# Kernel tuning notes

Hardware: AMD Instinct MI355X
Metric: run time of the kernel (lower is better)

Reference implementation:

```python
import math
import jax, jax.numpy as jnp
import numpy as np

B, L, DM = 2, 1024, 1024
STATE, EXPAND, CONV, DTR = 16, 2, 4, 8
INNER = DM * EXPAND          # 2048
NFFT = L // 2 + 1            # 513


def _silu(v):
    return v * jax.nn.sigmoid(v)


def setup_inputs() -> dict:
    key = jax.random.key(0)
    ks = jax.random.split(key, 12)
    s = lambda k, shape, sc=0.02: (jax.random.normal(k, shape, jnp.float32) * sc)
    # dt_proj bias initialized like the torch module: exp(U(0,1)*(log dt_max - log dt_min) + log dt_min)
    inv_dt = jnp.exp(jax.random.uniform(ks[10], (INNER,), jnp.float32)
                     * (math.log(0.1) - math.log(0.001)) + math.log(0.001))
    return {
        "x": jax.random.normal(ks[0], (B, L, DM), jnp.float32),
        "in_proj_w": s(ks[1], (2 * INNER, DM)),
        "conv_w": s(ks[2], (INNER, 1, CONV), 0.1),      # depthwise conv kernel
        "conv_b": jnp.zeros((INNER,), jnp.float32),
        "A_log": jnp.tile(jnp.log(jnp.arange(1, STATE + 1, dtype=jnp.float32)), (INNER, 1)),
        "D": jnp.ones((INNER,), jnp.float32),
        "x_proj_w": s(ks[3], (DTR + 2 * STATE, INNER)),
        "dt_proj_w": s(ks[4], (INNER, DTR)),
        "dt_proj_b": inv_dt,
        "filter_real": s(ks[5], (INNER, NFFT)),
        "filter_imag": s(ks[6], (INNER, NFFT)),
        "spectral_decay": jnp.ones((INNER,), jnp.float32) * 0.01,
        "fusion_w": s(ks[7], (INNER, 2 * INNER)),
        "fusion_b": jnp.zeros((INNER,), jnp.float32),
        "out_proj_w": s(ks[8], (DM, INNER)),
        "ln_gamma": jnp.ones((DM,), jnp.float32),
        "ln_beta": jnp.zeros((DM,), jnp.float32),
    }


def reference(x, in_proj_w, conv_w, conv_b, A_log, D, x_proj_w, dt_proj_w, dt_proj_b,
              filter_real, filter_imag, spectral_decay, fusion_w, fusion_b,
              out_proj_w, ln_gamma, ln_beta):
    residual = x
    xz = x @ in_proj_w.T                                   # [B,L,2*INNER]
    x_inner, z = xz[..., :INNER], xz[..., INNER:]
    z = _silu(z)

    # ---- SSM path ----
    xc = jnp.swapaxes(x_inner, 1, 2)                       # [B,E,L]
    xc = jax.lax.conv_general_dilated(
        xc, conv_w, (1,), [(CONV - 1, 0)],                 # causal depthwise conv (pad-left == torch pad + truncate)
        dimension_numbers=("NCH", "OIH", "NCH"),
        feature_group_count=INNER) + conv_b[None, :, None]
    x_conv = jnp.swapaxes(_silu(xc), 1, 2)                 # [B,L,E]

    x_dbc = x_conv @ x_proj_w.T                            # [B,L,DTR+2S]
    dt_x = x_dbc[..., :DTR]
    Bm = x_dbc[..., DTR:DTR + STATE]                       # [B,L,S]
    Cm = x_dbc[..., DTR + STATE:]                          # [B,L,S]
    dt = jax.nn.softplus(dt_x @ dt_proj_w.T + dt_proj_b)   # [B,L,E]
    A = -jnp.exp(A_log)                                    # [E,S]
    dA = jnp.exp(dt[..., None] * A)                        # [B,L,E,S]
    dBx = (dt * x_conv)[..., None] * Bm[:, :, None, :]     # [B,L,E,S]

    def step(h, inp):
        dA_t, dBx_t, C_t = inp
        h = dA_t * h + dBx_t                               # [B,E,S]
        return h, jnp.einsum('bes,bs->be', h, C_t)

    h0 = jnp.zeros((B, INNER, STATE), x.dtype)
    _, ys = jax.lax.scan(step, h0,
                         (jnp.swapaxes(dA, 0, 1), jnp.swapaxes(dBx, 0, 1), jnp.swapaxes(Cm, 0, 1)))
    y_ssm = jnp.swapaxes(ys, 0, 1) + x_conv * D            # [B,L,E]

    # ---- Spectral path ----
    xf = jnp.fft.rfft(jnp.swapaxes(x_inner, 1, 2), axis=-1)        # [B,E,NFFT]
    freqs = jnp.linspace(0.0, 1.0, NFFT)
    filt = (filter_real + 1j * filter_imag) * jnp.exp(-spectral_decay[:, None] * freqs[None, :])
    y_spec = jnp.swapaxes(jnp.fft.irfft(xf * filt[None], n=L, axis=-1), 1, 2)  # [B,L,E]

    # ---- Gated fusion ----
    g = jax.nn.sigmoid(jnp.concatenate([y_ssm, y_spec], -1) @ fusion_w.T + fusion_b)
    y = g * y_ssm + (1.0 - g) * y_spec
    y = y * z
    out = y @ out_proj_w.T + residual                      # [B,L,DM]

    mu = out.mean(-1, keepdims=True)
    var = out.var(-1, keepdims=True)
    return (out - mu) / jnp.sqrt(var + 1e-5) * ln_gamma + ln_beta
```

## Files before the change

### kernel.cpp

```cpp
#include <hip/hip_runtime.h>
#include <math.h>

#define B_ 2
#define L_ 1024
#define DM_ 1024
#define STATE_ 16
#define CONV_ 4
#define DTR_ 8
#define INNER_ 2048
#define M_ (B_*L_)
#define MD_ (B_*INNER_)
#define NFFT_ 513
#define NFP_ 1088
#define NCH_ 32
#define CHL_ 32
#define SK_ 16
#define KSL_ (2048/SK_)

typedef unsigned short u16;
typedef __attribute__((ext_vector_type(8))) short short8;
typedef __attribute__((ext_vector_type(8))) __bf16 bf16x8;
typedef __attribute__((ext_vector_type(4))) float f32x4;

__device__ __forceinline__ float frcp_(float x) { return __builtin_amdgcn_rcpf(x); }
__device__ __forceinline__ float fexp_(float x) { return __expf(x); }
__device__ __forceinline__ float fsigm_(float x) { return frcp_(1.f + __expf(-x)); }
__device__ __forceinline__ float fsilu_(float x) { return x * frcp_(1.f + __expf(-x)); }
__device__ __forceinline__ float fsoftplus_(float v) {
  return (v > 20.f) ? v : __logf(1.f + __expf(v));
}
__device__ __forceinline__ u16 f2bf(float f) {
  union { float f; unsigned u; } v; v.f = f;
  unsigned r = v.u + 0x7fffu + ((v.u >> 16) & 1u);
  return (u16)(r >> 16);
}
__device__ __forceinline__ float bf2f(u16 h) {
  union { unsigned u; float f; } v; v.u = ((unsigned)h) << 16;
  return v.f;
}
__device__ __forceinline__ void gload16(const void* g, void* l) {
  __builtin_amdgcn_global_load_lds(
      (const __attribute__((address_space(1))) unsigned*)g,
      (__attribute__((address_space(3))) unsigned*)l, 16, 0, 0);
}
__device__ __forceinline__ f32x4 mfma_bf16(short8 a, short8 b, f32x4 c) {
  return __builtin_amdgcn_mfma_f32_16x16x32_bf16(
      __builtin_bit_cast(bf16x8, a), __builtin_bit_cast(bf16x8, b), c, 0, 0, 0);
}

#define CVT2_N0 2097152
#define CVT2_NT 6291456
__global__ __launch_bounds__(256) void cvt2_k(
    const float* __restrict__ s0, const float* __restrict__ s1,
    u16* __restrict__ out)
{
  int i = (blockIdx.x*256 + threadIdx.x) * 4;
  const float* src; int off;
  if (i < CVT2_N0) { src = s0; off = 0; }
  else             { src = s1; off = CVT2_N0; }
  float4 v = *(const float4*)(src + (i - off));
  ushort4 o;
  o.x = f2bf(v.x); o.y = f2bf(v.y); o.z = f2bf(v.z); o.w = f2bf(v.w);
  *(ushort4*)(out + i) = o;
}

__device__ __forceinline__ void cvt16_body(int eb, int nthr, int t,
    const float* __restrict__ src, u16* __restrict__ dst)
{
  int i = (eb*nthr + t)*16;
  #pragma unroll
  for (int q = 0; q < 4; q++) {
    float4 v = *(const float4*)(src + i + q*4);
    ushort4 o;
    o.x = f2bf(v.x); o.y = f2bf(v.y); o.z = f2bf(v.z); o.w = f2bf(v.w);
    *(ushort4*)(dst + i + q*4) = o;
  }
}

__device__ __forceinline__ void conv_xt_body(int idx, const float* __restrict__ xz,
    const float* __restrict__ cw, const float* __restrict__ cb,
    float* __restrict__ xc, u16* __restrict__ xt)
{
  int c = idx & (INNER_-1);
  int g = idx >> 11;
  int b = g >> 7;
  int lb = (g & 127) * 8;
  float w0=cw[c*4+0], w1=cw[c*4+1], w2=cw[c*4+2], w3=cw[c*4+3];
  float bias = cb[c];
  float v[11];
  #pragma unroll
  for (int j = 0; j < 11; j++) {
    int l = lb - 3 + j;
    v[j] = (l >= 0) ? xz[((size_t)((b << 10) + l))*4096 + c] : 0.f;
  }
  union { u16 a[8]; short8 v8; } tu;
  #pragma unroll
  for (int j = 0; j < 8; j++) tu.a[j] = f2bf(v[j+3]);
  *(short8*)&xt[(((size_t)(b*INNER_ + c)) << 10) + lb] = tu.v8;
  #pragma unroll
  for (int j = 0; j < 8; j++) {
    float s = bias + w0*v[j] + w1*v[j+1] + w2*v[j+2] + w3*v[j+3];
    xc[((size_t)((b << 10) + lb + j))*INNER_ + c] = fsilu_(s);
  }
}

__device__ __forceinline__ void genWdft_body(int idx, u16* __restrict__ W)
{
  int l = idx & (L_-1);
  int col = idx >> 10;
  float v = 0.f;
  int f = col >> 1;
  if (f < NFFT_) {
    int ph = (l*f) & (L_-1);
    float th = (float)ph * (6.283185307179586f / (float)L_);
    v = (col & 1) ? -__sinf(th) : __cosf(th);
  }
  W[idx] = f2bf(v);
}

__device__ __forceinline__ void genWinv_body(int idx, u16* __restrict__ W)
{
  int r = idx % NFP_;
  int l = idx / NFP_;
  int f = r >> 1;
  float v = 0.f;
  if (f < NFFT_) {
    bool edge = (f == 0) || (f == 512);
    float sc = (edge ? 1.f : 2.f) / (float)L_;
    int ph = (f*l) & (L_-1);
    float th = (float)ph * (6.283185307179586f / (float)L_);
    if (r & 1) v = edge ? 0.f : -sc*__sinf(th);
    else       v = sc*__cosf(th);
  }
  W[idx] = f2bf(v);
}

__device__ __forceinline__ void xproj_body(int eb,
    const float* __restrict__ xconv, const float* __restrict__ W,
    float* __restrict__ part)
{
  const int sk = eb & (SK_-1), mt = eb / SK_;
  const int k0 = sk*KSL_;
  const int m = mt*256 + threadIdx.x;
  const float* arow = xconv + (size_t)m*2048 + k0;
  const float* wrow = W + k0;
  float acc[40];
  #pragma unroll
  for (int j=0;j<40;j++) acc[j]=0.f;
  for (int k = 0; k < KSL_; k += 4) {
    float4 a = *(const float4*)(arow + k);
    #pragma unroll
    for (int j = 0; j < 40; j++) {
      float4 b = *(const float4*)(wrow + (size_t)j*2048 + k);
      acc[j] += a.x*b.x + a.y*b.y + a.z*b.z + a.w*b.w;
    }
  }
  float* o = part + ((size_t)sk*M_ + m)*40;
  #pragma unroll
  for (int j = 0; j < 10; j++)
    *(float4*)(o + j*4) = make_float4(acc[j*4], acc[j*4+1], acc[j*4+2], acc[j*4+3]);
}

__device__ __forceinline__ void xpred_body(int i, const float* __restrict__ part,
                                           float* __restrict__ xdbc)
{
  float s = 0.f;
  #pragma unroll
  for (int sk = 0; sk < SK_; sk++) s += part[(size_t)sk*81920 + i];
  xdbc[i] = s;
}

__global__ __launch_bounds__(256) void aux2_k(
    const float* __restrict__ xz, const float* __restrict__ cw,
    const float* __restrict__ cb, float* __restrict__ xc,
    u16* __restrict__ xt, u16* __restrict__ Winv,
    const float* __restrict__ ows, u16* __restrict__ owd)
{
  int eb = blockIdx.x;
  if (eb < 2048)      conv_xt_body(eb*256 + threadIdx.x, xz, cw, cb, xc, xt);
  else if (eb < 6400) genWinv_body((eb - 2048)*256 + threadIdx.x, Winv);
  else                cvt16_body(eb - 6400, 256, threadIdx.x, ows, owd);
}

template<int TM, int TN, int EPI, int YCH, int AUX, int KS>
__global__ __launch_bounds__((TM/64)*(TN/32)*64) void mgemm_k(
    const u16* __restrict__ Ab, const u16* __restrict__ Bb,
    void* __restrict__ Cout, int K, int ldc,
    const float* __restrict__ aux0, u16* __restrict__ aux1,
    const float* __restrict__ aux2, const float* __restrict__ aux3,
    int gx, int gy,
    const float* __restrict__ ga, const float* __restrict__ gb,
    float* __restrict__ go, u16* __restrict__ gw,
    int ldk, const float* __restrict__ cvs, u16* __restrict__ cvd)
{
  constexpr int WN   = TN/32;
  constexpr int NW   = (TM/64)*WN;
  constexpr int NTHR = NW*64;
  __shared__ __align__(16) u16 As[2][TM*64];
  __shared__ __align__(16) u16 Bs[2][TN*64];
  const int t = threadIdx.x;
  const int nwg = gx * gy;

  if constexpr (AUX != 0) {
    int eb = (int)blockIdx.x - nwg*KS;
    if (eb >= 0) {
      if constexpr (AUX == 1) {
        if (eb < 2176) genWdft_body(eb*NTHR + t, gw);
        else           cvt16_body(eb - 2176, NTHR, t, cvs, cvd);
      } else if constexpr (AUX == 3) {
        xproj_body(eb, ga, gb, go);
      } else {
        xpred_body(eb*256 + t, ga, go);
      }
      return;
    }
  }

  const int lane = t & 63;
  const int w = t >> 6;
  const int wm = w / WN, wn = w % WN;

  int bid = blockIdx.x;
  int ks = 0;
  if constexpr (KS > 1) { ks = bid / nwg; bid -= ks*nwg; }
  const int k0 = ks * K;
  const int lid = (bid & 7) * (nwg >> 3) + (bid >> 3);
  int bx, by;
  if (YCH) { by = lid / gx; bx = lid - by*gx; }
  else     { bx = lid / gy; by = lid - bx*gy; }
  const int M0 = by * TM, N0 = bx * TN;

  f32x4 acc[4][2] = {};

  auto stage = [&](int buf, int kk0) {
    #pragma unroll
    for (int q = 0; q < TM*8/NTHR; q++) {
      int u = q*NTHR + t;
      int row = u >> 3, gpr = u & 7;
      int grp = gpr ^ (row & 7);
      gload16(Ab + (size_t)(M0+row)*ldk + k0 + kk0 + grp*8, &As[buf][u*8]);
    }
    #pragma unroll
    for (int q = 0; q < TN*8/NTHR; q++) {
      int u = q*NTHR + t;
      int row = u >> 3, gpr = u & 7;
      int grp = gpr ^ (row & 7);
      gload16(Bb + (size_t)(N0+row)*ldk + k0 + kk0 + grp*8, &Bs[buf][u*8]);
    }
  };

  stage(0, 0);
  const int nk = K >> 6;
  for (int kst = 0; kst < nk; kst++) {
    const int buf = kst & 1;
    __syncthreads();
    if (kst + 1 < nk) stage(buf ^ 1, (kst + 1) << 6);
    const u16* Asb = As[buf];
    const u16* Bsb = Bs[buf];
    #pragma unroll
    for (int kk = 0; kk < 2; kk++) {
      const int quad = lane >> 4;
      const int grp = kk*4 + quad;
      short8 af[4], bfr[2];
      #pragma unroll
      for (int i = 0; i < 4; i++) {
        int row = wm*64 + i*16 + (lane & 15);
        af[i] = *(const short8*)&Asb[(row*8 + (grp ^ (row & 7)))*8];
      }
      #pragma unroll
      for (int j = 0; j < 2; j++) {
        int row = wn*32 + j*16 + (lane & 15);
        bfr[j] = *(const short8*)&Bsb[(row*8 + (grp ^ (row & 7)))*8];
      }
      #pragma unroll
      for (int i = 0; i < 4; i++)
        #pragma unroll
        for (int j = 0; j < 2; j++)
          acc[i][j] = mfma_bf16(af[i], bfr[j], acc[i][j]);
    }
  }

  if constexpr (EPI == 6) {
    u16* T = (u16*)&As[0][0];
    __syncthreads();
    #pragma unroll
    for (int i = 0; i < 4; i++) {
      int cb = wm*64 + i*16 + (lane >> 4)*4;
      #pragma unroll
      for (int j = 0; j < 2; j++) {
        int ll = wn*32 + j*16 + (lane & 15);
        #pragma unroll
        for (int r = 0; r < 4; r++)
          T[(cb + r)*66 + ll] = f2bf(acc[i][j][r]);
      }
    }
    __syncthreads();
    const int b2 = M0 >> 11, c0 = M0 & (INNER_-1);
    u16* yc = (u16*)Cout;
    #pragma unroll
    for (int q = 0; q < (TM*TN/8)/NTHR; q++) {
      int task = q*NTHR + t;
      int cg = task & 15, ll = task >> 4;
      union { u16 a[8]; short8 v8; } tu;
      #pragma unroll
      for (int e = 0; e < 8; e++) tu.a[e] = T[(cg*8 + e)*66 + ll];
      *(short8*)&yc[((size_t)((b2 << 10) + N0 + ll) << 12) + 2048 + c0 + cg*8] = tu.v8;
    }
  } else {
    #pragma unroll
    for (int i = 0; i < 4; i++) {
      int mbase = M0 + wm*64 + i*16 + (lane >> 4)*4;
      #pragma unroll
      for (int j = 0; j < 2; j++) {
        int n = N0 + wn*32 + j*16 + (lane & 15);
        #pragma unroll
        for (int r = 0; r < 4; r++) {
          int m = mbase + r;
          float v = acc[i][j][r];
          if (EPI == 0) {
            ((float*)Cout)[(size_t)m*ldc + n] = v;
          } else if (EPI == 3) {
            float pv = __shfl_xor(v, 1, 64);
            int f = n >> 1;
            float outv = 0.f;
            if (f < NFFT_) {
              int c = m & (INNER_-1);
              float d  = fexp_(-aux2[c] * (float)f * (1.f/512.f));
              float wr = aux0[c*NFFT_+f]*d, wi = aux3[c*NFFT_+f]*d;
              float a = (n & 1) ? pv : v;
              float b = (n & 1) ? v : pv;
              outv = (n & 1) ? (a*wi + b*wr) : (a*wr - b*wi);
            }
            ((u16*)Cout)[(size_t)m*ldc + n] = f2bf(outv);
          } else if (EPI == 7) {
            float* P = (float*)Cout + (size_t)ks * ((size_t)gy*TM*ldc);
            P[(size_t)m*ldc + n] = v;
          } else {
            u16* P = (u16*)Cout + (size_t)ks * ((size_t)gy*TM*ldc);
            P[(size_t)m*ldc + n] = f2bf(v);
          }
        }
      }
    }
  }
}

__global__ __launch_bounds__(256) void combine_gate_k(
    const u16* __restrict__ P, const float* __restrict__ fus_b,
    const u16* __restrict__ ycat, const float* __restrict__ xz,
    u16* __restrict__ ycomb)
{
  int i4 = (blockIdx.x*256 + threadIdx.x)*4;
  int m = i4 >> 11, n = i4 & 2047;
  ushort4 p0 = *(const ushort4*)(P + i4);
  ushort4 p1 = *(const ushort4*)(P + 4194304 + i4);
  ushort4 ysv = *(const ushort4*)(ycat + (size_t)m*4096 + n);
  ushort4 ypv = *(const ushort4*)(ycat + (size_t)m*4096 + 2048 + n);
  float4 zv = *(const float4*)(xz + (size_t)m*4096 + 2048 + n);
  float4 fb = *(const float4*)(fus_b + n);
  float pp[4] = {bf2f(p0.x)+bf2f(p1.x), bf2f(p0.y)+bf2f(p1.y),
                 bf2f(p0.z)+bf2f(p1.z), bf2f(p0.w)+bf2f(p1.w)};
  float zz[4] = {zv.x, zv.y, zv.z, zv.w};
  float bb[4] = {fb.x, fb.y, fb.z, fb.w};
  u16 ys[4] = {ysv.x, ysv.y, ysv.z, ysv.w};
  u16 yp[4] = {ypv.x, ypv.y, ypv.z, ypv.w};
  ushort4 o;
  u16* op = (u16*)&o;
  #pragma unroll
  for (int j = 0; j < 4; j++) {
    float g = fsigm_(pp[j] + bb[j]);
    op[j] = f2bf((g*bf2f(ys[j]) + (1.f-g)*bf2f(yp[j]))*fsilu_(zz[j]));
  }
  *(ushort4*)(ycomb + i4) = o;
}

__global__ __launch_bounds__(256) void scan1_k(
    const float* __restrict__ xdbc, const float* __restrict__ xconv,
    const float* __restrict__ A_log, const float* __restrict__ dtw,
    const float* __restrict__ dtb, float* __restrict__ Pq)
{
  int idx = blockIdx.x*256 + threadIdx.x;
  int e  = idx & (INNER_-1);
  int bc = idx >> 11;
  int ch = bc & (NCH_-1);
  int b  = bc >> 5;
  float A[STATE_];
  #pragma unroll
  for (int s=0;s<STATE_;s++) A[s] = -fexp_(A_log[e*STATE_+s]);
  float w[DTR_];
  #pragma unroll
  for (int r=0;r<DTR_;r++) w[r] = dtw[e*DTR_+r];
  float bias = dtb[e];
  float h[STATE_] = {};
  float sdt = 0.f;
  int mbase = b*L_ + ch*CHL_;
  float dtx[DTR_], Bv[STATE_], xcv;
  {
    const float* row = xdbc + (size_t)mbase*40;
    #pragma unroll
    for (int r=0;r<DTR_;r++) dtx[r] = row[r];
    #pragma unroll
    for (int s=0;s<STATE_;s++) Bv[s] = row[8+s];
    xcv = xconv[(size_t)mbase*INNER_ + e];
  }
  for (int l=0;l<CHL_;l++) {
    float ndtx[DTR_], nBv[STATE_], nxcv = 0.f;
    if (l+1 < CHL_) {
      const float* nrow = xdbc + (size_t)(mbase+l+1)*40;
      #pragma unroll
      for (int r=0;r<DTR_;r++) ndtx[r] = nrow[r];
      #pragma unroll
      for (int s=0;s<STATE_;s++) nBv[s] = nrow[8+s];
      nxcv = xconv[(size_t)(mbase+l+1)*INNER_ + e];
    } else {
      #pragma unroll
      for (int r=0;r<DTR_;r++) ndtx[r] = 0.f;
      #pragma unroll
      for (int s=0;s<STATE_;s++) nBv[s] = 0.f;
    }
    float v = bias;
    #pragma unroll
    for (int r=0;r<DTR_;r++) v += dtx[r]*w[r];
    float dt = fsoftplus_(v);
    sdt += dt;
    float dx = dt * xcv;
    #pragma unroll
    for (int s=0;s<STATE_;s++) {
      float dA = fexp_(dt*A[s]);
      h[s] = dA*h[s] + dx*Bv[s];
    }
    #pragma unroll
    for (int r=0;r<DTR_;r++) dtx[r] = ndtx[r];
    #pragma unroll
    for (int s=0;s<STATE_;s++) Bv[s] = nBv[s];
    xcv = nxcv;
  }
  float* o = Pq + (size_t)idx*32;
  #pragma unroll
  for (int s=0;s<STATE_;s++) { o[s] = fexp_(A[s]*sdt); o[16+s] = h[s]; }
}

__global__ __launch_bounds__(256) void scan2_k(float* __restrict__ Pq)
{
  int idx = blockIdx.x*256 + threadIdx.x;
  int s = idx & 15;
  int e = (idx >> 4) & (INNER_-1);
  int b = idx >> 15;
  float h = 0.f;
  for (int ch = 0; ch < NCH_; ch++) {
    size_t base = ((size_t)(b*NCH_+ch)*INNER_ + e)*32;
    float p = Pq[base + s];
    float q = Pq[base + 16 + s];
    Pq[base + 16 + s] = h;
    h = p*h + q;
  }
}

__global__ __launch_bounds__(256) void scan3_k(
    const float* __restrict__ xdbc, const float* __restrict__ xconv,
    const float* __restrict__ A_log, const float* __restrict__ dtw,
    const float* __restrict__ dtb, const float* __restrict__ Dp,
    const float* __restrict__ Pq, u16* __restrict__ ycat)
{
  int idx = blockIdx.x*256 + threadIdx.x;
  int e  = idx & (INNER_-1);
  int bc = idx >> 11;
  int ch = bc & (NCH_-1);
  int b  = bc >> 5;
  float A[STATE_];
  #pragma unroll
  for (int s=0;s<STATE_;s++) A[s] = -fexp_(A_log[e*STATE_+s]);
  float w[DTR_];
  #pragma unroll
  for (int r=0;r<DTR_;r++) w[r] = dtw[e*DTR_+r];
  float bias = dtb[e];
  float Dv = Dp[e];
  float h[STATE_];
  const float* hi = Pq + (size_t)idx*32 + 16;
  #pragma unroll
  for (int s=0;s<STATE_;s++) h[s] = hi[s];
  int mbase = b*L_ + ch*CHL_;
  float dtx[DTR_], Bv[STATE_], Cv[STATE_], xcv;
  {
    const float* row = xdbc + (size_t)mbase*40;
    #pragma unroll
    for (int r=0;r<DTR_;r++) dtx[r] = row[r];
    #pragma unroll
    for (int s=0;s<STATE_;s++) { Bv[s] = row[8+s]; Cv[s] = row[24+s]; }
    xcv = xconv[(size_t)mbase*INNER_ + e];
  }
  for (int l=0;l<CHL_;l++) {
    float ndtx[DTR_], nBv[STATE_], nCv[STATE_], nxcv = 0.f;
    if (l+1 < CHL_) {
      const float* nrow = xdbc + (size_t)(mbase+l+1)*40;
      #pragma unroll
      for (int r=0;r<DTR_;r++) ndtx[r] = nrow[r];
      #pragma unroll
      for (int s=0;s<STATE_;s++) { nBv[s] = nrow[8+s]; nCv[s] = nrow[24+s]; }
      nxcv = xconv[(size_t)(mbase+l+1)*INNER_ + e];
    } else {
      #pragma unroll
      for (int r=0;r<DTR_;r++) ndtx[r] = 0.f;
      #pragma unroll
      for (int s=0;s<STATE_;s++) { nBv[s] = 0.f; nCv[s] = 0.f; }
    }
    float v = bias;
    #pragma unroll
    for (int r=0;r<DTR_;r++) v += dtx[r]*w[r];
    float dt = fsoftplus_(v);
    float dx = dt * xcv;
    float y = 0.f;
    #pragma unroll
    for (int s=0;s<STATE_;s++) {
      float dA = fexp_(dt*A[s]);
      h[s] = dA*h[s] + dx*Bv[s];
      y += h[s]*Cv[s];
    }
    ycat[(size_t)(mbase+l)*4096 + e] = f2bf(y + xcv*Dv);
    #pragma unroll
    for (int r=0;r<DTR_;r++) dtx[r] = ndtx[r];
    #pragma unroll
    for (int s=0;s<STATE_;s++) { Bv[s] = nBv[s]; Cv[s] = nCv[s]; }
    xcv = nxcv;
  }
}

__global__ __launch_bounds__(256) void ln2_k(const float* __restrict__ Q,
    const float* __restrict__ xres,
    const float* __restrict__ gma, const float* __restrict__ bta,
    float* __restrict__ out)
{
  int m = blockIdx.x;
  float s=0.f, s2=0.f;
  float v[4];
  #pragma unroll
  for (int j=0;j<4;j++) {
    int n = threadIdx.x + j*256;
    size_t idx = (size_t)m*DM_ + n;
    v[j] = Q[idx] + Q[2097152 + idx] + xres[idx];
    s += v[j]; s2 += v[j]*v[j];
  }
  #pragma unroll
  for (int off=32; off>=1; off>>=1) {
    s  += __shfl_down(s, off);
    s2 += __shfl_down(s2, off);
  }
  __shared__ float rs[4], rs2[4], stats[2];
  int wid = threadIdx.x >> 6;
  if ((threadIdx.x & 63) == 0) { rs[wid]=s; rs2[wid]=s2; }
  __syncthreads();
  if (threadIdx.x == 0) {
    float ts  = rs[0]+rs[1]+rs[2]+rs[3];
    float ts2 = rs2[0]+rs2[1]+rs2[2]+rs2[3];
    float mu  = ts/(float)DM_;
    float var = ts2/(float)DM_ - mu*mu;
    stats[0] = mu; stats[1] = rsqrtf(var + 1e-5f);
  }
  __syncthreads();
  float mu = stats[0], rstd = stats[1];
  #pragma unroll
  for (int j=0;j<4;j++) {
    int n = threadIdx.x + j*256;
    out[(size_t)m*DM_ + n] = (v[j]-mu)*rstd*gma[n] + bta[n];
  }
}

extern "C" void kernel_launch(void* const* d_in, const int* in_sizes, int n_in,
                              void* d_out, int out_size, void* d_ws, size_t ws_size,
                              hipStream_t stream)
{
  const float* x       = (const float*)d_in[0];
  const float* in_w    = (const float*)d_in[1];
  const float* conv_w  = (const float*)d_in[2];
  const float* conv_b  = (const float*)d_in[3];
  const float* A_log   = (const float*)d_in[4];
  const float* Dp      = (const float*)d_in[5];
  const float* xproj_w = (const float*)d_in[6];
  const float* dt_w    = (const float*)d_in[7];
  const float* dt_b    = (const float*)d_in[8];
  const float* f_re    = (const float*)d_in[9];
  const float* f_im    = (const float*)d_in[10];
  const float* s_dec   = (const float*)d_in[11];
  const float* fus_w   = (const float*)d_in[12];
  const float* fus_b   = (const float*)d_in[13];
  const float* out_w   = (const float*)d_in[14];
  const float* ln_g    = (const float*)d_in[15];
  const float* ln_b    = (const float*)d_in[16];
  float* out = (float*)d_out;

  float* ws    = (float*)d_ws;
  float* xz    = ws;
  float* xconv = xz    + 8388608;
  float* xdbc  = xconv + 4194304;
  float* Pq    = xdbc  + 81920;
  u16* ub      = (u16*)(Pq + 4194304);
  u16* xb      = ub;
  u16* inwb    = xb    + 2097152;
  u16* fuswb   = inwb  + 4194304;
  u16* outwb   = fuswb + 8388608;
  u16* xt      = outwb + 2097152;
  u16* Wb      = xt    + 4194304;
  u16* XFb     = Wb    + 1114112;
  u16* ycat    = XFb   + 4456448;
  u16* ycomb   = xt;
  u16* Winv    = xb;
  float* part  = (float*)inwb;
  u16* fpart   = (u16*)xconv;
  float* opart = Pq;

  cvt2_k<<<CVT2_NT/1024, 256, 0, stream>>>(x, in_w, xb);

  mgemm_k<128,128,0,0,1,1><<<512 + 2176 + 1024, 512, 0, stream>>>(
      xb, inwb, xz, 1024, 4096, nullptr, nullptr, nullptr, nullptr, 32, 16,
      nullptr, nullptr, nullptr, Wb, 1024, fus_w, fuswb);
  aux2_k<<<6912, 256, 0, stream>>>(xz, conv_w, conv_b, xconv, xt, Winv, out_w, outwb);
  mgemm_k<128,64,3,1,3,1><<<544 + SK_*8, 256, 0, stream>>>(
      xt, Wb, XFb, 1024, NFP_, f_re, nullptr, s_dec, f_im, 17, 32,
      xconv, xproj_w, part, nullptr, 1024, nullptr, nullptr);
  mgemm_k<128,64,6,1,4,1><<<512 + 320, 256, 0, stream>>>(
      XFb, Winv, ycat, NFP_, 0, nullptr, nullptr, nullptr, nullptr, 16, 32,
      part, nullptr, xdbc, nullptr, NFP_, nullptr, nullptr);
  scan1_k<<<(B_*NCH_*INNER_)/256, 256, 0, stream>>>(xdbc, xconv, A_log, dt_w, dt_b, Pq);
  scan2_k<<<(B_*INNER_*STATE_)/256, 256, 0, stream>>>(Pq);
  scan3_k<<<(B_*NCH_*INNER_)/256, 256, 0, stream>>>(xdbc, xconv, A_log, dt_w, dt_b, Dp, Pq, ycat);
  mgemm_k<128,128,8,0,0,2><<<2*256, 512, 0, stream>>>(
      ycat, fuswb, fpart, 2048, 2048, nullptr, nullptr, nullptr, nullptr, 16, 16,
      nullptr, nullptr, nullptr, nullptr, 4096, nullptr, nullptr);
  combine_gate_k<<<(2048*2048/4)/256, 256, 0, stream>>>(
      fpart, fus_b, ycat, xz, ycomb);
  mgemm_k<64,64,7,1,0,2><<<2*512, 128, 0, stream>>>(
      ycomb, outwb, opart, 1024, 1024, nullptr, nullptr, nullptr, nullptr, 16, 32,
      nullptr, nullptr, nullptr, nullptr, 2048, nullptr, nullptr);
  ln2_k<<<M_, 256, 0, stream>>>(opart, x, ln_g, ln_b, out);
}
```

Before: 399.1 us.

## Compute x_proj with bf16 MFMA GEMM instead of fp32 split-K scalar path

```diff
diff --git a/kernel.cpp b/kernel.cpp
--- a/kernel.cpp
+++ b/kernel.cpp
@@ -14,8 +14,6 @@
 #define NFP_ 1088
 #define NCH_ 32
 #define CHL_ 32
-#define SK_ 16
-#define KSL_ (2048/SK_)
 
 typedef unsigned short u16;
 typedef __attribute__((ext_vector_type(8))) short short8;
@@ -135,51 +133,18 @@
   W[idx] = f2bf(v);
 }
 
-__device__ __forceinline__ void xproj_body(int eb,
-    const float* __restrict__ xconv, const float* __restrict__ W,
-    float* __restrict__ part)
-{
-  const int sk = eb & (SK_-1), mt = eb / SK_;
-  const int k0 = sk*KSL_;
-  const int m = mt*256 + threadIdx.x;
-  const float* arow = xconv + (size_t)m*2048 + k0;
-  const float* wrow = W + k0;
-  float acc[40];
-  #pragma unroll
-  for (int j=0;j<40;j++) acc[j]=0.f;
-  for (int k = 0; k < KSL_; k += 4) {
-    float4 a = *(const float4*)(arow + k);
-    #pragma unroll
-    for (int j = 0; j < 40; j++) {
-      float4 b = *(const float4*)(wrow + (size_t)j*2048 + k);
-      acc[j] += a.x*b.x + a.y*b.y + a.z*b.z + a.w*b.w;
-    }
-  }
-  float* o = part + ((size_t)sk*M_ + m)*40;
-  #pragma unroll
-  for (int j = 0; j < 10; j++)
-    *(float4*)(o + j*4) = make_float4(acc[j*4], acc[j*4+1], acc[j*4+2], acc[j*4+3]);
-}
-
-__device__ __forceinline__ void xpred_body(int i, const float* __restrict__ part,
-                                           float* __restrict__ xdbc)
-{
-  float s = 0.f;
-  #pragma unroll
-  for (int sk = 0; sk < SK_; sk++) s += part[(size_t)sk*81920 + i];
-  xdbc[i] = s;
-}
-
 __global__ __launch_bounds__(256) void aux2_k(
     const float* __restrict__ xz, const float* __restrict__ cw,
     const float* __restrict__ cb, float* __restrict__ xc,
     u16* __restrict__ xt, u16* __restrict__ Winv,
-    const float* __restrict__ ows, u16* __restrict__ owd)
+    const float* __restrict__ ows, u16* __restrict__ owd,
+    const float* __restrict__ xpws, u16* __restrict__ xpwd)
 {
   int eb = blockIdx.x;
   if (eb < 2048)      conv_xt_body(eb*256 + threadIdx.x, xz, cw, cb, xc, xt);
   else if (eb < 6400) genWinv_body((eb - 2048)*256 + threadIdx.x, Winv);
-  else                cvt16_body(eb - 6400, 256, threadIdx.x, ows, owd);
+  else if (eb < 6912) cvt16_body(eb - 6400, 256, threadIdx.x, ows, owd);
+  else                cvt16_body(eb - 6912, 256, threadIdx.x, xpws, xpwd);
 }
 
 template<int TM, int TN, int EPI, int YCH, int AUX, int KS>
@@ -189,8 +154,7 @@
     const float* __restrict__ aux0, u16* __restrict__ aux1,
     const float* __restrict__ aux2, const float* __restrict__ aux3,
     int gx, int gy,
-    const float* __restrict__ ga, const float* __restrict__ gb,
-    float* __restrict__ go, u16* __restrict__ gw,
+    u16* __restrict__ gw,
     int ldk, const float* __restrict__ cvs, u16* __restrict__ cvd)
 {
   constexpr int WN   = TN/32;
@@ -207,10 +171,8 @@
       if constexpr (AUX == 1) {
         if (eb < 2176) genWdft_body(eb*NTHR + t, gw);
         else           cvt16_body(eb - 2176, NTHR, t, cvs, cvd);
-      } else if constexpr (AUX == 3) {
-        xproj_body(eb, ga, gb, go);
       } else {
-        xpred_body(eb*256 + t, ga, go);
+        cvt16_body(eb, NTHR, t, cvs, cvd);
       }
       return;
     }
@@ -335,9 +297,11 @@
           } else if (EPI == 7) {
             float* P = (float*)Cout + (size_t)ks * ((size_t)gy*TM*ldc);
             P[(size_t)m*ldc + n] = v;
-          } else {
+          } else if (EPI == 8) {
             u16* P = (u16*)Cout + (size_t)ks * ((size_t)gy*TM*ldc);
             P[(size_t)m*ldc + n] = f2bf(v);
+          } else {
+            if (n < 40) ((float*)Cout)[(size_t)m*40 + n] = v;
           }
         }
       }
@@ -604,7 +568,8 @@
   u16* ycat    = XFb   + 4456448;
   u16* ycomb   = xt;
   u16* Winv    = xb;
-  float* part  = (float*)inwb;
+  u16* xpwb    = xb + 1114112;
+  u16* xcb     = inwb;
   u16* fpart   = (u16*)xconv;
   float* opart = Pq;
 
@@ -612,24 +577,28 @@
 
   mgemm_k<128,128,0,0,1,1><<<512 + 2176 + 1024, 512, 0, stream>>>(
       xb, inwb, xz, 1024, 4096, nullptr, nullptr, nullptr, nullptr, 32, 16,
-      nullptr, nullptr, nullptr, Wb, 1024, fus_w, fuswb);
-  aux2_k<<<6912, 256, 0, stream>>>(xz, conv_w, conv_b, xconv, xt, Winv, out_w, outwb);
-  mgemm_k<128,64,3,1,3,1><<<544 + SK_*8, 256, 0, stream>>>(
+      Wb, 1024, fus_w, fuswb);
+  aux2_k<<<6932, 256, 0, stream>>>(xz, conv_w, conv_b, xconv, xt, Winv,
+                                   out_w, outwb, xproj_w, xpwb);
+  mgemm_k<128,64,3,1,3,1><<<544 + 1024, 256, 0, stream>>>(
       xt, Wb, XFb, 1024, NFP_, f_re, nullptr, s_dec, f_im, 17, 32,
-      xconv, xproj_w, part, nullptr, 1024, nullptr, nullptr);
-  mgemm_k<128,64,6,1,4,1><<<512 + 320, 256, 0, stream>>>(
+      nullptr, 1024, xconv, xcb);
+  mgemm_k<128,64,9,1,0,1><<<16, 256, 0, stream>>>(
+      xcb, xpwb, xdbc, 2048, 40, nullptr, nullptr, nullptr, nullptr, 1, 16,
+      nullptr, 2048, nullptr, nullptr);
+  mgemm_k<128,64,6,1,0,1><<<512, 256, 0, stream>>>(
       XFb, Winv, ycat, NFP_, 0, nullptr, nullptr, nullptr, nullptr, 16, 32,
-      part, nullptr, xdbc, nullptr, NFP_, nullptr, nullptr);
+      nullptr, NFP_, nullptr, nullptr);
   scan1_k<<<(B_*NCH_*INNER_)/256, 256, 0, stream>>>(xdbc, xconv, A_log, dt_w, dt_b, Pq);
   scan2_k<<<(B_*INNER_*STATE_)/256, 256, 0, stream>>>(Pq);
   scan3_k<<<(B_*NCH_*INNER_)/256, 256, 0, stream>>>(xdbc, xconv, A_log, dt_w, dt_b, Dp, Pq, ycat);
   mgemm_k<128,128,8,0,0,2><<<2*256, 512, 0, stream>>>(
       ycat, fuswb, fpart, 2048, 2048, nullptr, nullptr, nullptr, nullptr, 16, 16,
-      nullptr, nullptr, nullptr, nullptr, 4096, nullptr, nullptr);
+      nullptr, 4096, nullptr, nullptr);
   combine_gate_k<<<(2048*2048/4)/256, 256, 0, stream>>>(
       fpart, fus_b, ycat, xz, ycomb);
   mgemm_k<64,64,7,1,0,2><<<2*512, 128, 0, stream>>>(
       ycomb, outwb, opart, 1024, 1024, nullptr, nullptr, nullptr, nullptr, 16, 32,
-      nullptr, nullptr, nullptr, nullptr, 2048, nullptr, nullptr);
+      nullptr, 2048, nullptr, nullptr);
   ln2_k<<<M_, 256, 0, stream>>>(opart, x, ln_g, ln_b, out);
 }
```

New measurement: 381.4 us. 4.4% less time.
